# Performance work log

Measured on AMD Instinct MI355X. Metric: run time of the kernel, lower is better.

The kernel has to match this reference:

```python
import jax, jax.numpy as jnp
import numpy as np

B, F, C = 16384, 256, 256


def setup_inputs() -> dict:
    key = jax.random.key(0)
    ks = jax.random.split(key, 10)
    return {
        "x_t": jax.random.normal(ks[0], (B, F), dtype=jnp.float32),
        "n_t": jax.random.normal(ks[1], (B, C), dtype=jnp.float32),
        "d_t": jax.random.uniform(ks[2], (B, C), dtype=jnp.float32),
        "h_t": jax.random.normal(ks[3], (B, C), dtype=jnp.float32),
        "a_max_t": jax.random.normal(ks[4], (B, C), dtype=jnp.float32),
        "Wu": jax.random.normal(ks[5], (C, F), dtype=jnp.float32) * 0.06,
        "bu": jnp.zeros((C,), dtype=jnp.float32),
        "Wg": jax.random.normal(ks[6], (C, F + C), dtype=jnp.float32) * 0.05,
        "bg": jnp.zeros((C,), dtype=jnp.float32),
        "Wa": jax.random.normal(ks[7], (C, F + C), dtype=jnp.float32) * 0.05,
        "Wd": jax.random.normal(ks[8], (C, F + C), dtype=jnp.float32) * 0.05,
    }


def reference(x_t, n_t, d_t, h_t, a_max_t, Wu, bu, Wg, bg, Wa, Wd):
    # xh_join = cat([x_t, h_t], dim=1) -> [B, F+C]
    xh = jnp.concatenate([x_t, h_t], axis=1)
    u_t = x_t @ Wu.T + bu                      # [B, C]
    g_t = xh @ Wg.T + bg                       # [B, C]
    a_t = xh @ Wa.T                            # [B, C] (no bias)
    z_t = u_t * jnp.tanh(g_t)
    # decay branch (self.decay is an nn.Linear -> always truthy in original)
    decay = jax.nn.sigmoid(xh @ Wd.T)
    e_neg = jnp.exp(-decay)
    a_decay = a_max_t * e_neg
    a_newmax = jnp.maximum(a_decay, a_t)
    exp_diff = jnp.exp(a_max_t - a_newmax)
    exp_scaled = jnp.exp(a_t - a_newmax)
    n_new = n_t * e_neg * exp_diff + z_t * exp_scaled
    d_new = d_t * e_neg * exp_diff + exp_scaled
    h_new = jnp.tanh(n_new / d_new)
    return (n_new, d_new, h_new, a_newmax)
```

## Files before the change

### kernel.cpp

```cpp
#include <hip/hip_runtime.h>

typedef _Float16 f16x8 __attribute__((ext_vector_type(8)));
typedef float f32x4 __attribute__((ext_vector_type(4)));

#define B_SZ 16384
#define C_SZ 256
#define BC (B_SZ * C_SZ)

__global__ __launch_bounds__(256) void pack_w(const float* __restrict__ Wu,
                                              const float* __restrict__ Wg,
                                              const float* __restrict__ Wa,
                                              const float* __restrict__ Wd,
                                              _Float16* __restrict__ wsB) {
  int tid = blockIdx.x * 256 + threadIdx.x;
  int k0 = (tid & 63) * 8;
  int p = tid >> 6;
  int cb = p >> 8;
  int r = p & 255;
  int wv = r >> 6;
  int strip = (r >> 4) & 3;
  int t = r & 15;
  int c = cb * 64 + wv * 16 + t;
  float v[8];
  if (strip == 0) {
    if (k0 < 256) {
      const float* s = Wu + c * 256 + k0;
#pragma unroll
      for (int i = 0; i < 8; ++i) v[i] = s[i];
    } else {
#pragma unroll
      for (int i = 0; i < 8; ++i) v[i] = 0.f;
    }
  } else {
    const float* s = (strip == 1 ? Wg : (strip == 2 ? Wa : Wd)) + c * 512 + k0;
#pragma unroll
    for (int i = 0; i < 8; ++i) v[i] = s[i];
  }
  f16x8 o;
#pragma unroll
  for (int i = 0; i < 8; ++i) o[i] = (_Float16)v[i];
  *reinterpret_cast<f16x8*>(wsB + (size_t)p * 512 + k0) = o;
}

__global__ __launch_bounds__(256, 2) void rwa_main(
    const float* __restrict__ x, const float* __restrict__ nt_,
    const float* __restrict__ dt_, const float* __restrict__ h,
    const float* __restrict__ amax_, const float* __restrict__ bu,
    const float* __restrict__ bg, const _Float16* __restrict__ wsB,
    float* __restrict__ out) {
  __shared__ __align__(16) _Float16 ldsA[2][64 * 64];
  __shared__ __align__(16) _Float16 ldsB[2][256 * 64];

  const int tid = threadIdx.x;
  const int lane = tid & 63;
  const int wv = tid >> 6;

  const int bid = blockIdx.x;
  const int xcd = bid & 7;
  const int q = bid >> 3;
  const int cb = q & 3;
  const int rowblk = (q >> 2) * 8 + xcd;
  const int row0 = rowblk * 64;

  const int sr = tid >> 3;
  const int scf = (tid & 7) * 8;

  f32x4 acc[4][4] = {};

  auto stageA = [&](int buf, int kt) {
    const float* src = (kt < 4) ? x : h;
    const int kcol = (kt & 3) * 64;
#pragma unroll
    for (int s = 0; s < 2; ++s) {
      const int r = s * 32 + sr;
      const float* sp = src + (size_t)(row0 + r) * 256 + kcol + scf;
      f32x4 a0 = *reinterpret_cast<const f32x4*>(sp);
      f32x4 a1 = *reinterpret_cast<const f32x4*>(sp + 4);
      f16x8 o;
#pragma unroll
      for (int i = 0; i < 4; ++i) { o[i] = (_Float16)a0[i]; o[4 + i] = (_Float16)a1[i]; }
      const int off = (r * 128 + scf * 2) ^ ((r & 7) << 4);
      *reinterpret_cast<f16x8*>(reinterpret_cast<char*>(&ldsA[buf][0]) + off) = o;
    }
  };

  auto stageB = [&](int buf, int kt) {
#pragma unroll
    for (int s = 0; s < 8; ++s) {
      const int r = s * 32 + sr;
      const _Float16* sp = wsB + (size_t)(cb * 256 + r) * 512 + kt * 64 + scf;
      f16x8 vv = *reinterpret_cast<const f16x8*>(sp);
      const int off = (r * 128 + scf * 2) ^ ((r & 7) << 4);
      *reinterpret_cast<f16x8*>(reinterpret_cast<char*>(&ldsB[buf][0]) + off) = vv;
    }
  };

  stageA(0, 0);
  stageB(0, 0);
  __syncthreads();

  const int l15 = lane & 15;
  const int lg = lane >> 4;
  const int swz = (lane & 7) << 4;

  int buf = 0;
  for (int kt = 0; kt < 8; ++kt) {
    if (kt < 7) {
      stageA(buf ^ 1, kt + 1);
      stageB(buf ^ 1, kt + 1);
    }
    const char* pA = reinterpret_cast<const char*>(&ldsA[buf][0]);
    const char* pB = reinterpret_cast<const char*>(&ldsB[buf][0]);
    const bool doU = (kt < 4);
#pragma unroll
    for (int ks = 0; ks < 2; ++ks) {
      f16x8 af[4];
#pragma unroll
      for (int mi = 0; mi < 4; ++mi) {
        const int row = mi * 16 + l15;
        af[mi] = *reinterpret_cast<const f16x8*>(
            pA + ((row * 128 + ks * 64 + lg * 16) ^ swz));
      }
      f16x8 bfr[4];
#pragma unroll
      for (int ni = 0; ni < 4; ++ni) {
        if (ni == 0 && !doU) continue;
        const int row = wv * 64 + ni * 16 + l15;
        bfr[ni] = *reinterpret_cast<const f16x8*>(
            pB + ((row * 128 + ks * 64 + lg * 16) ^ swz));
      }
#pragma unroll
      for (int ni = 0; ni < 4; ++ni) {
        if (ni == 0 && !doU) continue;
#pragma unroll
        for (int mi = 0; mi < 4; ++mi)
          acc[mi][ni] = __builtin_amdgcn_mfma_f32_16x16x32_f16(
              af[mi], bfr[ni], acc[mi][ni], 0, 0, 0);
      }
    }
    __syncthreads();
    buf ^= 1;
  }

  const int c = cb * 64 + wv * 16 + l15;
  const float buv = bu[c];
  const float bgv = bg[c];
  const int rbase = row0 + lg * 4;
#pragma unroll
  for (int mi = 0; mi < 4; ++mi) {
#pragma unroll
    for (int rg = 0; rg < 4; ++rg) {
      const int r = rbase + mi * 16 + rg;
      const int idx = r * 256 + c;
      const float u = acc[mi][0][rg] + buv;
      const float g = acc[mi][1][rg] + bgv;
      const float a = acc[mi][2][rg];
      const float dr = acc[mi][3][rg];
      const float decay = 1.f / (1.f + __expf(-dr));
      const float e_neg = __expf(-decay);
      const float z = u * tanhf(g);
      const float am = amax_[idx];
      const float n_old = nt_[idx];
      const float d_old = dt_[idx];
      const float a_dec = am * e_neg;
      const float a_new = fmaxf(a_dec, a);
      const float ediff = __expf(am - a_new);
      const float escal = __expf(a - a_new);
      const float comm = e_neg * ediff;
      const float n_new = n_old * comm + z * escal;
      const float d_new = d_old * comm + escal;
      const float h_new = tanhf(n_new / d_new);
      out[idx] = n_new;
      out[BC + idx] = d_new;
      out[2 * BC + idx] = h_new;
      out[3 * BC + idx] = a_new;
    }
  }
}

extern "C" void kernel_launch(void* const* d_in, const int* in_sizes, int n_in,
                              void* d_out, int out_size, void* d_ws, size_t ws_size,
                              hipStream_t stream) {
  const float* x_t    = (const float*)d_in[0];
  const float* n_t    = (const float*)d_in[1];
  const float* d_t    = (const float*)d_in[2];
  const float* h_t    = (const float*)d_in[3];
  const float* amax_t = (const float*)d_in[4];
  const float* Wu     = (const float*)d_in[5];
  const float* bu     = (const float*)d_in[6];
  const float* Wg     = (const float*)d_in[7];
  const float* bg     = (const float*)d_in[8];
  const float* Wa     = (const float*)d_in[9];
  const float* Wd     = (const float*)d_in[10];
  float* out = (float*)d_out;

  _Float16* wsB = (_Float16*)d_ws;

  pack_w<<<256, 256, 0, stream>>>(Wu, Wg, Wa, Wd, wsB);
  rwa_main<<<1024, 256, 0, stream>>>(x_t, n_t, d_t, h_t, amax_t, bu, bg, wsB, out);
}
```

Before: 57.96 us.

## Load weight fragments directly from global and register-prefetch A tiles

Removes the LDS staging buffer for the packed weight matrix, so each wave reads its B fragments straight from global memory (L2-resident) into registers. The A tile is now prefetched into registers before the MFMAs and written to the other LDS buffer afterwards, using hand-placed waitcnt and barrier instructions instead of __syncthreads. The much smaller shared-memory footprint allows raising the occupancy hint to 3 blocks per CU. The trade-off is more global/L2 traffic for weights, since each of the four waves fetches its own fragments, and higher register pressure that may cause spills.

```diff
diff --git a/kernel.cpp b/kernel.cpp
--- a/kernel.cpp
+++ b/kernel.cpp
@@ -42,18 +42,19 @@
   *reinterpret_cast<f16x8*>(wsB + (size_t)p * 512 + k0) = o;
 }
 
-__global__ __launch_bounds__(256, 2) void rwa_main(
+__global__ __launch_bounds__(256, 3) void rwa_main(
     const float* __restrict__ x, const float* __restrict__ nt_,
     const float* __restrict__ dt_, const float* __restrict__ h,
     const float* __restrict__ amax_, const float* __restrict__ bu,
     const float* __restrict__ bg, const _Float16* __restrict__ wsB,
     float* __restrict__ out) {
   __shared__ __align__(16) _Float16 ldsA[2][64 * 64];
-  __shared__ __align__(16) _Float16 ldsB[2][256 * 64];
 
   const int tid = threadIdx.x;
   const int lane = tid & 63;
   const int wv = tid >> 6;
+  const int l15 = lane & 15;
+  const int lg = lane >> 4;
 
   const int bid = blockIdx.x;
   const int xcd = bid & 7;
@@ -62,56 +63,62 @@
   const int rowblk = (q >> 2) * 8 + xcd;
   const int row0 = rowblk * 64;
 
-  const int sr = tid >> 3;
-  const int scf = (tid & 7) * 8;
+  const int sr = tid >> 2;
+  const int sk = (tid & 3) * 16;
+  const float* xrow = x + (size_t)(row0 + sr) * 256 + sk;
+  const float* hrow = h + (size_t)(row0 + sr) * 256 + sk;
+  const int wswz = (sr & 7) << 4;
+  const int wo = sr * 128 + sk * 2;
+
+  const int rswz = (l15 & 7) << 4;
+
+  const _Float16* bbase = wsB + (size_t)(cb * 256 + wv * 64 + l15) * 512;
 
   f32x4 acc[4][4] = {};
-
-  auto stageA = [&](int buf, int kt) {
-    const float* src = (kt < 4) ? x : h;
-    const int kcol = (kt & 3) * 64;
-#pragma unroll
-    for (int s = 0; s < 2; ++s) {
-      const int r = s * 32 + sr;
-      const float* sp = src + (size_t)(row0 + r) * 256 + kcol + scf;
-      f32x4 a0 = *reinterpret_cast<const f32x4*>(sp);
-      f32x4 a1 = *reinterpret_cast<const f32x4*>(sp + 4);
-      f16x8 o;
-#pragma unroll
-      for (int i = 0; i < 4; ++i) { o[i] = (_Float16)a0[i]; o[4 + i] = (_Float16)a1[i]; }
-      const int off = (r * 128 + scf * 2) ^ ((r & 7) << 4);
-      *reinterpret_cast<f16x8*>(reinterpret_cast<char*>(&ldsA[buf][0]) + off) = o;
-    }
+  f32x4 ar[4];
+
+  auto issueA = [&](int kt) {
+    const float* sp = (kt < 4 ? xrow : hrow) + (kt & 3) * 64;
+#pragma unroll
+    for (int i = 0; i < 4; ++i) ar[i] = *reinterpret_cast<const f32x4*>(sp + i * 4);
   };
-
-  auto stageB = [&](int buf, int kt) {
-#pragma unroll
-    for (int s = 0; s < 8; ++s) {
-      const int r = s * 32 + sr;
-      const _Float16* sp = wsB + (size_t)(cb * 256 + r) * 512 + kt * 64 + scf;
-      f16x8 vv = *reinterpret_cast<const f16x8*>(sp);
-      const int off = (r * 128 + scf * 2) ^ ((r & 7) << 4);
-      *reinterpret_cast<f16x8*>(reinterpret_cast<char*>(&ldsB[buf][0]) + off) = vv;
-    }
+  auto writeA = [&](int buf) {
+    f16x8 o0, o1;
+#pragma unroll
+    for (int i = 0; i < 4; ++i) {
+      o0[i] = (_Float16)ar[0][i];
+      o0[4 + i] = (_Float16)ar[1][i];
+      o1[i] = (_Float16)ar[2][i];
+      o1[4 + i] = (_Float16)ar[3][i];
+    }
+    char* pW = reinterpret_cast<char*>(&ldsA[buf][0]);
+    *reinterpret_cast<f16x8*>(pW + (wo ^ wswz)) = o0;
+    *reinterpret_cast<f16x8*>(pW + ((wo + 16) ^ wswz)) = o1;
   };
 
-  stageA(0, 0);
-  stageB(0, 0);
-  __syncthreads();
-
-  const int l15 = lane & 15;
-  const int lg = lane >> 4;
-  const int swz = (lane & 7) << 4;
-
-  int buf = 0;
+  issueA(0);
+  writeA(0);
+  asm volatile("s_waitcnt lgkmcnt(0)" ::: "memory");
+  __builtin_amdgcn_s_barrier();
+  __builtin_amdgcn_sched_barrier(0);
+
+#pragma unroll
   for (int kt = 0; kt < 8; ++kt) {
-    if (kt < 7) {
-      stageA(buf ^ 1, kt + 1);
-      stageB(buf ^ 1, kt + 1);
-    }
+    const int buf = kt & 1;
+    const bool doU = (kt < 4);
+
+    f16x8 bfr[2][4];
+#pragma unroll
+    for (int ks = 0; ks < 2; ++ks)
+#pragma unroll
+      for (int ni = 0; ni < 4; ++ni)
+        if (ni > 0 || doU)
+          bfr[ks][ni] = *reinterpret_cast<const f16x8*>(
+              bbase + ni * (16 * 512) + kt * 64 + ks * 32 + lg * 8);
+
+    if (kt < 7) issueA(kt + 1);
+
     const char* pA = reinterpret_cast<const char*>(&ldsA[buf][0]);
-    const char* pB = reinterpret_cast<const char*>(&ldsB[buf][0]);
-    const bool doU = (kt < 4);
 #pragma unroll
     for (int ks = 0; ks < 2; ++ks) {
       f16x8 af[4];
@@ -119,27 +126,24 @@
       for (int mi = 0; mi < 4; ++mi) {
         const int row = mi * 16 + l15;
         af[mi] = *reinterpret_cast<const f16x8*>(
-            pA + ((row * 128 + ks * 64 + lg * 16) ^ swz));
+            pA + ((row * 128 + ks * 64 + lg * 16) ^ rswz));
       }
-      f16x8 bfr[4];
 #pragma unroll
       for (int ni = 0; ni < 4; ++ni) {
         if (ni == 0 && !doU) continue;
-        const int row = wv * 64 + ni * 16 + l15;
-        bfr[ni] = *reinterpret_cast<const f16x8*>(
-            pB + ((row * 128 + ks * 64 + lg * 16) ^ swz));
-      }
-#pragma unroll
-      for (int ni = 0; ni < 4; ++ni) {
-        if (ni == 0 && !doU) continue;
 #pragma unroll
         for (int mi = 0; mi < 4; ++mi)
           acc[mi][ni] = __builtin_amdgcn_mfma_f32_16x16x32_f16(
-              af[mi], bfr[ni], acc[mi][ni], 0, 0, 0);
+              af[mi], bfr[ks][ni], acc[mi][ni], 0, 0, 0);
       }
     }
-    __syncthreads();
-    buf ^= 1;
+
+    if (kt < 7) {
+      writeA(buf ^ 1);
+      asm volatile("s_waitcnt lgkmcnt(0)" ::: "memory");
+      __builtin_amdgcn_s_barrier();
+      __builtin_amdgcn_sched_barrier(0);
+    }
   }
 
   const int c = cb * 64 + wv * 16 + l15;
```

New measurement: 74.95 us. 1.29x slower.
